# Kernel optimization log

Measured on AMD Instinct MI355X. Metric: run time of the kernel, lower is better.

The kernel has to match this reference:

```python
import jax, jax.numpy as jnp
import numpy as np

R, MAXI, MAXO = 333, 119, 12   # n ROIs, max roi input size, max roi reduced size
E, H = 3328, 8                  # embed dim (concat 3325 + pad 3), heads
HD = E // H                     # 416
CONCAT = 3325
EPS = 1e-5


def _roi_layout():
    """Deterministic synthetic ROI sizes + gather maps for vectorized ragged encode."""
    sizes = 30 + (7 * np.arange(R)) % 90            # per-ROI input widths
    reduced = 8 + np.arange(R) % 5                  # per-ROI output widths
    reduced[332] = 8                                # makes concat+3 divisible by 8
    starts = np.concatenate([[0], np.cumsum(sizes)[:-1]])
    total = int(sizes.sum())                        # 24696
    in_idx = np.minimum(starts[:, None] + np.arange(MAXI)[None, :], total - 1)
    in_mask = (np.arange(MAXI)[None, :] < sizes[:, None]).astype(np.float32)
    out_idx = np.concatenate([i * MAXO + np.arange(reduced[i]) for i in range(R)])
    assert out_idx.shape[0] == CONCAT
    return jnp.asarray(in_idx), jnp.asarray(in_mask), jnp.asarray(out_idx)


def _bn(x, g, b):
    # training-mode BatchNorm1d: biased batch stats (matches torch normalization)
    m = x.mean(0)
    v = x.var(0)
    return (x - m) * jax.lax.rsqrt(v + EPS) * g + b


def _lrelu(x, s):
    return jnp.where(x > 0, x, s * x)


def setup_inputs() -> dict:
    key = jax.random.key(0)
    ks = jax.random.split(key, 16)
    B, TOTAL = 2048, 24696
    f32 = jnp.float32
    return {
        'x': jax.random.normal(ks[0], (B, TOTAL), f32),
        'enc_W': jax.random.normal(ks[1], (R, MAXO, MAXI), f32) * 0.1,
        'enc_b': jax.random.normal(ks[2], (R, MAXO), f32) * 0.02,
        'bn1_g': jnp.ones((CONCAT,), f32),
        'bn1_b': jnp.zeros((CONCAT,), f32),
        'Wqkv': jax.random.normal(ks[3], (3 * E, E), f32) * (1.0 / np.sqrt(E)),
        'bqkv': jnp.zeros((3 * E,), f32),
        'Wo': jax.random.normal(ks[4], (E, E), f32) * (1.0 / np.sqrt(E)),
        'bo': jnp.zeros((E,), f32),
        'W1': jax.random.normal(ks[5], (1024, E), f32) * (1.0 / np.sqrt(E)),
        'b1': jnp.zeros((1024,), f32),
        'bn2_g': jnp.ones((1024,), f32),
        'bn2_b': jnp.zeros((1024,), f32),
        'W2': jax.random.normal(ks[6], (300, 1024), f32) * (1.0 / 32.0),
        'b2': jnp.zeros((300,), f32),
        'Wc': jax.random.normal(ks[7], (180, 300), f32) * 0.06,
        'bc': jnp.zeros((180,), f32),
    }


def reference(x, enc_W, enc_b, bn1_g, bn1_b, Wqkv, bqkv, Wo, bo,
              W1, b1, bn2_g, bn2_b, W2, b2, Wc, bc):
    in_idx, in_mask, out_idx = _roi_layout()
    B = x.shape[0]
    # --- vectorized ragged per-ROI Linear (replaces 333-way python loop) ---
    xp = x[:, in_idx] * in_mask                     # [B, R, MAXI], padded slices
    y = jnp.einsum('bri,roi->bro', xp, enc_W) + enc_b  # [B, R, MAXO]
    y = y.reshape(B, R * MAXO)[:, out_idx]          # ragged concat -> [B, 3325]
    # per-ROI BN+LeakyReLU(0.3) == per-feature on the concat
    y = _lrelu(_bn(y, bn1_g, bn1_b), 0.3)
    y = jnp.pad(y, ((0, 0), (1, 2)))                # F.pad (1, 2) -> [B, 3328]
    # --- MultiheadAttention, seq_len = 1 (input unsqueezed to [1, B, E]) ---
    qkv = y @ Wqkv.T + bqkv                         # [B, 3E]
    q, k, v = jnp.split(qkv, 3, axis=-1)
    q = q.reshape(B, H, 1, HD)
    k = k.reshape(B, H, 1, HD)
    v = v.reshape(B, H, 1, HD)
    s = jnp.einsum('bhqd,bhkd->bhqk', q, k) / jnp.sqrt(jnp.float32(HD))
    a = jax.nn.softmax(s, axis=-1)                  # trivially 1 for L=1, kept faithful
    o = jnp.einsum('bhqk,bhkd->bhqd', a, v).reshape(B, E)
    o = o @ Wo.T + bo
    r = _lrelu(_bn(o @ W1.T + b1, bn2_g, bn2_b), 0.1)
    reg_out = r @ W2.T + b2                         # [B, 300]
    y_pred = jax.nn.softmax(reg_out @ Wc.T + bc, axis=-1)  # [B, 180]
    return reg_out, y_pred
```

## Files before the change

kernel.cpp:

```cpp
#include <hip/hip_runtime.h>
#include <hip/hip_bf16.h>

#define B_      2048
#define R_      333
#define MAXI_   119
#define MAXO_   12
#define CONCAT_ 3325
#define E_      3328
#define TOTAL_  24696
#define HID_    1024
#define NREG_   300
#define NCLS_   180
#define EPS_    1e-5f
#define NSLOT_  128
#define PSTR_   3328
#define NS2_    128

typedef __attribute__((ext_vector_type(8))) short bf16x8;
typedef __attribute__((ext_vector_type(4))) float f32x4;

static __device__ inline unsigned short f2bf_rne(float f) {
  unsigned u;
  __builtin_memcpy(&u, &f, 4);
  u += 0x7fff + ((u >> 16) & 1);
  return (unsigned short)(u >> 16);
}
static __device__ inline float bf2f(unsigned short s) {
  unsigned u = (unsigned)s << 16;
  float f;
  __builtin_memcpy(&f, &u, 4);
  return f;
}

__global__ void layout_kernel(int* __restrict__ starts, int* __restrict__ red_starts) {
  if (threadIdx.x == 0 && blockIdx.x == 0) {
    int s = 0, rs = 0;
    for (int r = 0; r < R_; ++r) {
      starts[r] = s;
      red_starts[r] = rs;
      s += 30 + (7 * r) % 90;
      rs += (r == 332) ? 8 : (8 + r % 5);
    }
  }
}

__device__ __forceinline__ void rowdot_body(
    const float* __restrict__ A, const float* __restrict__ v, const float* __restrict__ b,
    float* __restrict__ out, int N, int K, int jb) {
  int wid = threadIdx.x >> 6, lane = threadIdx.x & 63;
  int j = jb * 4 + wid;
  if (j >= N) return;
  const float* row = A + (size_t)j * K;
  float s = 0.f;
  for (int k = lane; k < K; k += 64) s = fmaf(row[k], v[k], s);
  for (int o = 32; o; o >>= 1) s += __shfl_down(s, o);
  if (lane == 0) out[j] = s + b[j];
}

__device__ __forceinline__ void pack_w_body(const float* __restrict__ enc_W,
                                            const int* __restrict__ starts,
                                            unsigned short* __restrict__ Wpk, int r) {
  int tid = threadIdx.x;
  int kc = tid >> 6, lane = tid & 63;
  int size = 30 + (7 * r) % 90;
  int s8 = starts[r] & 7;
  int oc = lane & 15;
  int k0 = kc * 32 + (lane >> 4) * 8;
  unsigned short o[8];
#pragma unroll
  for (int e = 0; e < 8; ++e) {
    int k = k0 + e - s8;
    float v = 0.f;
    if (oc < MAXO_ && k >= 0 && k < size) v = enc_W[((size_t)r * MAXO_ + oc) * MAXI_ + k];
    o[e] = f2bf_rne(v);
  }
  unsigned short* dst = Wpk + ((size_t)r * 4 + kc) * 512 + lane * 8;
  *(ushort4*)dst = *(ushort4*)&o[0];
  *(ushort4*)(dst + 4) = *(ushort4*)&o[4];
}

__global__ __launch_bounds__(256) void packw_rd1_kernel(
    const float* __restrict__ enc_W, const int* __restrict__ starts,
    unsigned short* __restrict__ Wpk,
    const float* __restrict__ Wo, const float* __restrict__ bv,
    const float* __restrict__ bo, float* __restrict__ t1v) {
  int bid = blockIdx.x;
  if (bid < R_) pack_w_body(enc_W, starts, Wpk, bid);
  else          rowdot_body(Wo, bv, bo, t1v, E_, E_, bid - R_);
}

__device__ __forceinline__ void encode_body(
    const float* __restrict__ x, const unsigned short* __restrict__ Wpk,
    const float* __restrict__ enc_b, const int* __restrict__ starts,
    const int* __restrict__ red_starts,
    unsigned short* __restrict__ yT, float* __restrict__ pS1, float* __restrict__ pS2,
    int r, int bg) {
  int tid = threadIdx.x;
  int wid = tid >> 6, lane = tid & 63;
  int lr = lane & 15, kg = lane >> 4;

  int size = 30 + (7 * r) % 90;
  int red  = (r == 332) ? 8 : (8 + r % 5);
  int st   = starts[r];
  int s8   = st & 7;
  int a0   = st & ~7;
  int rs   = red_starts[r];
  int nkc  = (s8 + size + 31) >> 5;
  int kmax = TOTAL_ - a0;

  bf16x8 wf[4];
  const unsigned short* wp = Wpk + (size_t)r * 2048 + lane * 8;
#pragma unroll
  for (int kc = 0; kc < 4; ++kc) wf[kc] = *(const bf16x8*)(wp + kc * 512);

  float bofs[4];
#pragma unroll
  for (int reg = 0; reg < 4; ++reg) {
    int oc = kg * 4 + reg;
    bofs[reg] = (oc < MAXO_) ? enc_b[r * MAXO_ + oc] : 0.f;
  }

  for (int t = 0; t < 4; ++t) {
    int b0 = bg * 256 + wid * 64 + t * 16;
    const float* xrow = x + (size_t)(b0 + lr) * TOTAL_ + a0;
    f32x4 acc = {0.f, 0.f, 0.f, 0.f};
#pragma unroll
    for (int kc = 0; kc < 4; ++kc) {
      if (kc < nkc) {
        int k0 = kc * 32 + kg * 8;
        if (k0 + 8 > kmax) k0 = kmax - 8;
        float4 v0 = *(const float4*)(xrow + k0);
        float4 v1 = *(const float4*)(xrow + k0 + 4);
        bf16x8 xf;
        xf[0] = (short)f2bf_rne(v0.x); xf[1] = (short)f2bf_rne(v0.y);
        xf[2] = (short)f2bf_rne(v0.z); xf[3] = (short)f2bf_rne(v0.w);
        xf[4] = (short)f2bf_rne(v1.x); xf[5] = (short)f2bf_rne(v1.y);
        xf[6] = (short)f2bf_rne(v1.z); xf[7] = (short)f2bf_rne(v1.w);
        acc = __builtin_amdgcn_mfma_f32_16x16x32_bf16(wf[kc], xf, acc, 0, 0, 0);
      }
    }
    int slot = b0 >> 4;
#pragma unroll
    for (int reg = 0; reg < 4; ++reg) {
      int oc = kg * 4 + reg;
      if (oc < red) {
        float v = acc[reg] + bofs[reg];
        yT[(size_t)(rs + oc) * B_ + b0 + lr] = f2bf_rne(v);
        float a = v, s2 = v * v;
#pragma unroll
        for (int m = 1; m <= 8; m <<= 1) { a += __shfl_xor(a, m); s2 += __shfl_xor(s2, m); }
        if (lr == 0) {
          pS1[slot * PSTR_ + rs + oc] = a;
          pS2[slot * PSTR_ + rs + oc] = s2;
        }
      }
    }
  }
}

#define ENC_NB_ (R_ * 8)
#define NTR_    ((E_ / 64) * (E_ / 64))
#define NC4A_   (HID_ * E_ / 4)
#define NC4B_   (NREG_ * HID_ / 4)
#define NCAST_  ((NC4A_ + NC4B_ + 255) / 256)
__global__ __launch_bounds__(256) void grand_kernel(
    const float* __restrict__ x, const unsigned short* __restrict__ Wpk,
    const float* __restrict__ enc_b, const int* __restrict__ starts,
    const int* __restrict__ red_starts,
    unsigned short* __restrict__ yT, float* __restrict__ pS1, float* __restrict__ pS2,
    const float* __restrict__ Wo, const float* __restrict__ Wv,
    unsigned short* __restrict__ WoT, unsigned short* __restrict__ WvT,
    const float* __restrict__ W1, unsigned short* __restrict__ W1b,
    const float* __restrict__ W2, unsigned short* __restrict__ W2b,
    const float* __restrict__ t1v, const float* __restrict__ b1, float* __restrict__ zbv) {
  __shared__ float tile[64][65];
  int bid = blockIdx.x;
  if (bid < ENC_NB_) {
    encode_body(x, Wpk, enc_b, starts, red_starts, yT, pS1, pS2, bid >> 3, bid & 7);
  } else if (bid < ENC_NB_ + 2 * NTR_) {
    int tb = bid - ENC_NB_;
    int z = tb / NTR_, rem = tb % NTR_;
    const float* in = z ? Wv : Wo;
    unsigned short* out = z ? WvT : WoT;
    int c0 = (rem % 52) * 64, r0 = (rem / 52) * 64;
    int t = threadIdx.x;
    int ci = t & 63, ri0 = t >> 6;
    for (int ri = ri0; ri < 64; ri += 4)
      tile[ri][ci] = in[(size_t)(r0 + ri) * E_ + c0 + ci];
    __syncthreads();
    int rj = t & 63, i0 = t >> 6;
    for (int i = i0; i < 64; i += 4)
      out[(size_t)(c0 + i) * E_ + r0 + rj] = f2bf_rne(tile[rj][i]);
  } else if (bid < ENC_NB_ + 2 * NTR_ + NCAST_) {
    int i = (bid - ENC_NB_ - 2 * NTR_) * 256 + threadIdx.x;
    const float* src; unsigned short* dst; int idx;
    if (i < NC4A_) { src = W1; dst = W1b; idx = i; }
    else if (i < NC4A_ + NC4B_) { src = W2; dst = W2b; idx = i - NC4A_; }
    else return;
    float4 v = ((const float4*)src)[idx];
    ushort4 o;
    o.x = f2bf_rne(v.x); o.y = f2bf_rne(v.y); o.z = f2bf_rne(v.z); o.w = f2bf_rne(v.w);
    ((ushort4*)dst)[idx] = o;
  } else {
    rowdot_body(W1, t1v, b1, zbv, HID_, E_, bid - ENC_NB_ - 2 * NTR_ - NCAST_);
  }
}

template <int KS, bool OUT_BF16>
__device__ __forceinline__ void gemm_body(
    const unsigned short* __restrict__ A, const unsigned short* __restrict__ W,
    float* __restrict__ Cf, unsigned short* __restrict__ Cb,
    int M, int N, int K, int bx, int by, int bz, unsigned short* smem) {
  unsigned short* a_lds = smem;
  unsigned short* b_lds = smem + 8192;
  int tid = threadIdx.x;
  int wid = tid >> 6, lane = tid & 63;
  int wr = wid >> 1, wc = wid & 1;
  int row0 = by * 128, col0 = bx * 128;
  int lr = lane & 15, kg = lane >> 4;
  int Klocal = K / KS;
  int kbase = bz * Klocal;

  int srow = tid >> 2, sk = (tid & 3) * 8;
  const unsigned short* aptr0 = A + (size_t)(row0 + srow) * K + kbase + sk;
  const unsigned short* aptr1 = aptr0 + (size_t)64 * K;
  int bcol0 = col0 + srow;      if (bcol0 > N - 1) bcol0 = N - 1;
  int bcol1 = col0 + 64 + srow; if (bcol1 > N - 1) bcol1 = N - 1;
  const unsigned short* bptr0 = W + (size_t)bcol0 * K + kbase + sk;
  const unsigned short* bptr1 = W + (size_t)bcol1 * K + kbase + sk;

  f32x4 acc[4][4] = {};
  int nk = Klocal >> 5;

#define STAGE_(buf, kc)                                                                             \
  do {                                                                                              \
    __builtin_amdgcn_global_load_lds((const __attribute__((address_space(1))) void*)(aptr0 + (kc)), \
        (__attribute__((address_space(3))) void*)(a_lds + (buf) * 4096 + wid * 512), 16, 0, 0);     \
    __builtin_amdgcn_global_load_lds((const __attribute__((address_space(1))) void*)(aptr1 + (kc)), \
        (__attribute__((address_space(3))) void*)(a_lds + (buf) * 4096 + 2048 + wid * 512), 16, 0, 0); \
    __builtin_amdgcn_global_load_lds((const __attribute__((address_space(1))) void*)(bptr0 + (kc)), \
        (__attribute__((address_space(3))) void*)(b_lds + (buf) * 4096 + wid * 512), 16, 0, 0);     \
    __builtin_amdgcn_global_load_lds((const __attribute__((address_space(1))) void*)(bptr1 + (kc)), \
        (__attribute__((address_space(3))) void*)(b_lds + (buf) * 4096 + 2048 + wid * 512), 16, 0, 0); \
  } while (0)

  STAGE_(0, 0);
  __syncthreads();
  int cur = 0;
  for (int t = 0; t < nk; ++t) {
    if (t + 1 < nk) STAGE_(cur ^ 1, (t + 1) * 32);
    bf16x8 a[4], b[4];
#pragma unroll
    for (int f = 0; f < 4; ++f) {
      a[f] = *(const bf16x8*)(a_lds + cur * 4096 + (wr * 64 + f * 16 + lr) * 32 + kg * 8);
      b[f] = *(const bf16x8*)(b_lds + cur * 4096 + (wc * 64 + f * 16 + lr) * 32 + kg * 8);
    }
#pragma unroll
    for (int i = 0; i < 4; ++i)
#pragma unroll
      for (int j = 0; j < 4; ++j)
        acc[i][j] = __builtin_amdgcn_mfma_f32_16x16x32_bf16(a[i], b[j], acc[i][j], 0, 0, 0);
    __syncthreads();
    cur ^= 1;
  }
#undef STAGE_

#pragma unroll
  for (int j = 0; j < 4; ++j) {
    int ccol = col0 + wc * 64 + j * 16 + lr;
    if (ccol >= N) continue;
#pragma unroll
    for (int i = 0; i < 4; ++i) {
#pragma unroll
      for (int reg = 0; reg < 4; ++reg) {
        int crow = row0 + wr * 64 + i * 16 + kg * 4 + reg;
        float v = acc[i][j][reg];
        if (KS == 1) {
          if (OUT_BF16) Cb[(size_t)crow * N + ccol] = f2bf_rne(v);
          else          Cf[(size_t)crow * N + ccol] = v;
        } else {
          Cf[((size_t)bz * M + crow) * N + ccol] = v;
        }
      }
    }
  }
}

#define WA_NB_ ((E_ / 128) * (HID_ / 128))
__global__ __launch_bounds__(256) void wa_stats_kernel(
    const unsigned short* __restrict__ W1b, const unsigned short* __restrict__ WoT,
    unsigned short* __restrict__ Wa_bf,
    const float* __restrict__ pS1, const float* __restrict__ pS2,
    float* __restrict__ mean, float* __restrict__ rstd) {
  __shared__ __align__(16) unsigned short smem[16384];
  int bid = blockIdx.x;
  if (bid < WA_NB_) {
    gemm_body<1, true>(W1b, WoT, nullptr, Wa_bf, HID_, E_, E_,
                       bid % (E_ / 128), bid / (E_ / 128), 0, smem);
  } else {
    int c = (bid - WA_NB_) * 256 + threadIdx.x;
    if (c >= CONCAT_) return;
    float s = 0.f, s2 = 0.f;
    for (int i = 0; i < NSLOT_; ++i) { s += pS1[i * PSTR_ + c]; s2 += pS2[i * PSTR_ + c]; }
    float m = s / B_;
    float v = s2 / B_ - m * m;
    mean[c] = m;
    rstd[c] = rsqrtf(v + EPS_);
  }
}

#define TR_NB_ ((E_ / 64) * (B_ / 64))
__global__ __launch_bounds__(256) void trans_wb_kernel(
    const unsigned short* __restrict__ yT, const float* __restrict__ mean,
    const float* __restrict__ rstd, const float* __restrict__ g,
    const float* __restrict__ bb, unsigned short* __restrict__ Y,
    const unsigned short* __restrict__ Wa_bf, const unsigned short* __restrict__ WvT,
    unsigned short* __restrict__ Wb_bf) {
  __shared__ __align__(16) unsigned short smem[16384];
  int bid = blockIdx.x;
  if (bid < WA_NB_) {
    gemm_body<1, true>(Wa_bf, WvT, nullptr, Wb_bf, HID_, E_, E_,
                       bid % (E_ / 128), bid / (E_ / 128), 0, smem);
  } else {
    int tb = bid - WA_NB_;
    int cc0 = (tb % 52) * 64, b0 = (tb / 52) * 64;
    float (*tile)[65] = (float(*)[65])smem;
    int t = threadIdx.x;
    int bi = t & 63, ci0 = t >> 6;
    for (int ci = ci0; ci < 64; ci += 4) {
      int c = cc0 + ci - 1;
      float v = 0.f;
      if (c >= 0 && c < CONCAT_) {
        float f = bf2f(yT[(size_t)c * B_ + b0 + bi]);
        v = (f - mean[c]) * rstd[c] * g[c] + bb[c];
        v = v > 0.f ? v : 0.3f * v;
      }
      tile[ci][bi] = v;
    }
    __syncthreads();
    int cj = t & 63, bj0 = t >> 6;
    for (int bj = bj0; bj < 64; bj += 4)
      Y[(size_t)(b0 + bj) * E_ + cc0 + cj] = f2bf_rne(tile[cj][bj]);
  }
}

template <int KS, bool OUT_BF16>
__global__ __launch_bounds__(256) void gemm_kernel(
    const unsigned short* __restrict__ A, const unsigned short* __restrict__ W,
    float* __restrict__ Cf, unsigned short* __restrict__ Cb, int M, int N, int K) {
  __shared__ __align__(16) unsigned short smem[16384];
  gemm_body<KS, OUT_BF16>(A, W, Cf, Cb, M, N, K, blockIdx.x, blockIdx.y, blockIdx.z, smem);
}

__global__ __launch_bounds__(256) void combZ_stats_kernel(
    const float* __restrict__ Cpart, const float* __restrict__ zb,
    float* __restrict__ Z, float* __restrict__ pS, float* __restrict__ pS2) {
  int c = blockIdx.x * 256 + threadIdx.x;
  int ry = blockIdx.y;
  float zbc = zb[c];
  float s1 = 0.f, s2 = 0.f;
  for (int r = ry * 16; r < ry * 16 + 16; ++r) {
    float v = zbc;
#pragma unroll
    for (int z = 0; z < 4; ++z) v += Cpart[((size_t)z * B_ + r) * HID_ + c];
    Z[(size_t)r * HID_ + c] = v;
    s1 += v; s2 = fmaf(v, v, s2);
  }
  pS[ry * HID_ + c] = s1;
  pS2[ry * HID_ + c] = s2;
}

__global__ __launch_bounds__(256) void colstats_final_kernel(
    const float* __restrict__ pS, const float* __restrict__ pS2,
    float* __restrict__ mean, float* __restrict__ rstd) {
  int c = blockIdx.x * 256 + threadIdx.x;
  if (c >= HID_) return;
  float s = 0.f, s2 = 0.f;
  for (int i = 0; i < NS2_; ++i) { s += pS[i * HID_ + c]; s2 += pS2[i * HID_ + c]; }
  float m = s / B_;
  float v = s2 / B_ - m * m;
  mean[c] = m;
  rstd[c] = rsqrtf(v + EPS_);
}

__global__ __launch_bounds__(256) void bn2_apply_kernel(
    const float* __restrict__ Z, const float* __restrict__ mean, const float* __restrict__ rstd,
    const float* __restrict__ g, const float* __restrict__ bb, unsigned short* __restrict__ R) {
  int i = blockIdx.x * 256 + threadIdx.x;
  int c = i & (HID_ - 1);
  float v = (Z[i] - mean[c]) * rstd[c] * g[c] + bb[c];
  v = v > 0.f ? v : 0.1f * v;
  R[i] = f2bf_rne(v);
}

__global__ __launch_bounds__(256) void classifier_kernel(
    const float* __restrict__ Cpart, const float* __restrict__ b2,
    const float* __restrict__ Wc, const float* __restrict__ bc,
    float* __restrict__ reg_out, float* __restrict__ ypred) {
  int b = blockIdx.x;
  __shared__ __align__(16) float rrow[NREG_];
  __shared__ float sl[256];
  int tid = threadIdx.x;
  for (int i = tid; i < NREG_; i += 256) {
    float s = b2[i];
#pragma unroll
    for (int z = 0; z < 4; ++z) s += Cpart[((size_t)z * B_ + b) * NREG_ + i];
    rrow[i] = s;
    reg_out[(size_t)b * NREG_ + i] = s;
  }
  __syncthreads();
  float s = -1e30f;
  if (tid < NCLS_) {
    const float* w = Wc + (size_t)tid * NREG_;
    float acc = 0.f;
    for (int k = 0; k < NREG_; k += 4) {
      float4 wv = *(const float4*)(w + k);
      float4 rv = *(const float4*)(&rrow[k]);
      acc = fmaf(wv.x, rv.x, acc); acc = fmaf(wv.y, rv.y, acc);
      acc = fmaf(wv.z, rv.z, acc); acc = fmaf(wv.w, rv.w, acc);
    }
    s = acc + bc[tid];
  }
  sl[tid] = s;
  __syncthreads();
  for (int o = 128; o > 0; o >>= 1) {
    if (tid < o) sl[tid] = fmaxf(sl[tid], sl[tid + o]);
    __syncthreads();
  }
  float mx = sl[0];
  __syncthreads();
  float e = (tid < NCLS_) ? __expf(s - mx) : 0.f;
  sl[tid] = e;
  __syncthreads();
  for (int o = 128; o > 0; o >>= 1) {
    if (tid < o) sl[tid] += sl[tid + o];
    __syncthreads();
  }
  if (tid < NCLS_) ypred[(size_t)b * NCLS_ + tid] = e / sl[0];
}

extern "C" void kernel_launch(void* const* d_in, const int* in_sizes, int n_in,
                              void* d_out, int out_size, void* d_ws, size_t ws_size,
                              hipStream_t stream) {
  const float* x     = (const float*)d_in[0];
  const float* enc_W = (const float*)d_in[1];
  const float* enc_b = (const float*)d_in[2];
  const float* bn1_g = (const float*)d_in[3];
  const float* bn1_b = (const float*)d_in[4];
  const float* Wqkv  = (const float*)d_in[5];
  const float* bqkv  = (const float*)d_in[6];
  const float* Wo    = (const float*)d_in[7];
  const float* bo    = (const float*)d_in[8];
  const float* W1    = (const float*)d_in[9];
  const float* b1    = (const float*)d_in[10];
  const float* bn2_g = (const float*)d_in[11];
  const float* bn2_b = (const float*)d_in[12];
  const float* W2    = (const float*)d_in[13];
  const float* b2    = (const float*)d_in[14];
  const float* Wc    = (const float*)d_in[15];
  const float* bc    = (const float*)d_in[16];

  char* ws = (char*)d_ws;
  size_t off = 0;
  auto alloc = [&](size_t bytes) -> void* {
    void* p = ws + off;
    off += (bytes + 255) & ~(size_t)255;
    return p;
  };

  unsigned short* yT     = (unsigned short*)alloc((size_t)CONCAT_ * B_ * 2);
  float*          pS1b   = (float*)alloc((size_t)NSLOT_ * PSTR_ * 4);
  float*          pS2b   = (float*)alloc((size_t)NSLOT_ * PSTR_ * 4);
  float*          mean1  = (float*)alloc(CONCAT_ * 4);
  float*          rstd1  = (float*)alloc(CONCAT_ * 4);
  unsigned short* Ybf    = (unsigned short*)alloc((size_t)B_ * E_ * 2);
  unsigned short* Rbf    = (unsigned short*)alloc((size_t)B_ * HID_ * 2);
  unsigned short* WoT_bf = (unsigned short*)alloc((size_t)E_ * E_ * 2);
  unsigned short* WvT_bf = (unsigned short*)alloc((size_t)E_ * E_ * 2);
  unsigned short* W1_bf  = (unsigned short*)alloc((size_t)HID_ * E_ * 2);
  unsigned short* W2_bf  = (unsigned short*)alloc((size_t)NREG_ * HID_ * 2);
  unsigned short* Wa_bf  = (unsigned short*)alloc((size_t)HID_ * E_ * 2);
  unsigned short* Wb_bf  = (unsigned short*)alloc((size_t)HID_ * E_ * 2);
  unsigned short* Wpk    = (unsigned short*)alloc((size_t)R_ * 2048 * 2);
  float*          Cpart  = (float*)alloc((size_t)4 * B_ * HID_ * 4);
  float*          t1v    = (float*)alloc(E_ * 4);
  float*          zbv    = (float*)alloc(HID_ * 4);
  float*          partS  = (float*)alloc((size_t)NS2_ * HID_ * 4);
  float*          partS2 = (float*)alloc((size_t)NS2_ * HID_ * 4);
  float*          mean2  = (float*)alloc(HID_ * 4);
  float*          rstd2  = (float*)alloc(HID_ * 4);
  int*            starts = (int*)alloc(R_ * 4);
  int*            redst  = (int*)alloc(R_ * 4);

  float* Z = (float*)yT;

  layout_kernel<<<1, 1, 0, stream>>>(starts, redst);
  packw_rd1_kernel<<<R_ + E_ / 4, 256, 0, stream>>>(
      enc_W, starts, Wpk, Wo, bqkv + 2 * E_, bo, t1v);
  grand_kernel<<<ENC_NB_ + 2 * NTR_ + NCAST_ + HID_ / 4, 256, 0, stream>>>(
      x, Wpk, enc_b, starts, redst, yT, pS1b, pS2b,
      Wo, Wqkv + (size_t)2 * E_ * E_, WoT_bf, WvT_bf,
      W1, W1_bf, W2, W2_bf, t1v, b1, zbv);
  wa_stats_kernel<<<WA_NB_ + (CONCAT_ + 255) / 256, 256, 0, stream>>>(
      W1_bf, WoT_bf, Wa_bf, pS1b, pS2b, mean1, rstd1);
  trans_wb_kernel<<<WA_NB_ + TR_NB_, 256, 0, stream>>>(
      yT, mean1, rstd1, bn1_g, bn1_b, Ybf, Wa_bf, WvT_bf, Wb_bf);
  gemm_kernel<4, false><<<dim3(HID_ / 128, B_ / 128, 4), 256, 0, stream>>>(
      Ybf, Wb_bf, Cpart, nullptr, B_, HID_, E_);
  combZ_stats_kernel<<<dim3(HID_ / 256, NS2_), 256, 0, stream>>>(Cpart, zbv, Z, partS, partS2);
  colstats_final_kernel<<<(HID_ + 255) / 256, 256, 0, stream>>>(partS, partS2, mean2, rstd2);
  bn2_apply_kernel<<<(B_ * HID_) / 256, 256, 0, stream>>>(Z, mean2, rstd2, bn2_g, bn2_b, Rbf);
  gemm_kernel<4, false><<<dim3((NREG_ + 127) / 128, B_ / 128, 4), 256, 0, stream>>>(
      Rbf, W2_bf, Cpart, nullptr, B_, NREG_, HID_);
  float* reg_out = (float*)d_out;
  classifier_kernel<<<B_, 256, 0, stream>>>(
      Cpart, b2, Wc, bc, reg_out, reg_out + (size_t)B_ * NREG_);
}
```

Baseline: 351.0 us.

## Reschedule kernel stages to overlap encode with weight-fold GEMM and split-K Wb

Weight transposes, casts and packing move into one prep kernel. The ROI encode now runs in the same launch as the Wa = W1·Wo fold GEMM, so the memory-bound encode overlaps the compute-bound GEMM. The encode no longer writes per-slot partial BN statistics; instead the column statistics are recomputed by reading yT back, in the same launch as a split-K (2-way) Wb GEMM. A later kernel sums the two Wb partials to bf16 alongside the transpose. The trade is an extra read of yT and extra fp32 partial traffic for Wb, in exchange for better concurrency and fewer partial-stat writes.

```diff
diff --git a/kernel.cpp b/kernel.cpp
--- a/kernel.cpp
+++ b/kernel.cpp
@@ -12,8 +12,6 @@
 #define NREG_   300
 #define NCLS_   180
 #define EPS_    1e-5f
-#define NSLOT_  128
-#define PSTR_   3328
 #define NS2_    128
 
 typedef __attribute__((ext_vector_type(8))) short bf16x8;
@@ -79,22 +77,55 @@
   *(ushort4*)(dst + 4) = *(ushort4*)&o[4];
 }
 
-__global__ __launch_bounds__(256) void packw_rd1_kernel(
+#define NTR_    ((E_ / 64) * (E_ / 64))
+#define NC4A_   (HID_ * E_ / 4)
+#define NC4B_   (NREG_ * HID_ / 4)
+#define NCAST_  ((NC4A_ + NC4B_ + 255) / 256)
+__global__ __launch_bounds__(256) void prep_kernel(
+    const float* __restrict__ Wo, const float* __restrict__ Wv,
+    unsigned short* __restrict__ WoT, unsigned short* __restrict__ WvT,
+    const float* __restrict__ W1, unsigned short* __restrict__ W1b,
+    const float* __restrict__ W2, unsigned short* __restrict__ W2b,
+    const float* __restrict__ bv, const float* __restrict__ bo, float* __restrict__ t1v,
     const float* __restrict__ enc_W, const int* __restrict__ starts,
-    unsigned short* __restrict__ Wpk,
-    const float* __restrict__ Wo, const float* __restrict__ bv,
-    const float* __restrict__ bo, float* __restrict__ t1v) {
+    unsigned short* __restrict__ Wpk) {
+  __shared__ float tile[64][65];
   int bid = blockIdx.x;
-  if (bid < R_) pack_w_body(enc_W, starts, Wpk, bid);
-  else          rowdot_body(Wo, bv, bo, t1v, E_, E_, bid - R_);
+  if (bid < 2 * NTR_) {
+    int z = bid / NTR_, rem = bid % NTR_;
+    const float* in = z ? Wv : Wo;
+    unsigned short* out = z ? WvT : WoT;
+    int c0 = (rem % 52) * 64, r0 = (rem / 52) * 64;
+    int t = threadIdx.x;
+    int ci = t & 63, ri0 = t >> 6;
+    for (int ri = ri0; ri < 64; ri += 4)
+      tile[ri][ci] = in[(size_t)(r0 + ri) * E_ + c0 + ci];
+    __syncthreads();
+    int rj = t & 63, i0 = t >> 6;
+    for (int i = i0; i < 64; i += 4)
+      out[(size_t)(c0 + i) * E_ + r0 + rj] = f2bf_rne(tile[rj][i]);
+  } else if (bid < 2 * NTR_ + NCAST_) {
+    int i = (bid - 2 * NTR_) * 256 + threadIdx.x;
+    const float* src; unsigned short* dst; int idx;
+    if (i < NC4A_) { src = W1; dst = W1b; idx = i; }
+    else if (i < NC4A_ + NC4B_) { src = W2; dst = W2b; idx = i - NC4A_; }
+    else return;
+    float4 v = ((const float4*)src)[idx];
+    ushort4 o;
+    o.x = f2bf_rne(v.x); o.y = f2bf_rne(v.y); o.z = f2bf_rne(v.z); o.w = f2bf_rne(v.w);
+    ((ushort4*)dst)[idx] = o;
+  } else if (bid < 2 * NTR_ + NCAST_ + E_ / 4) {
+    rowdot_body(Wo, bv, bo, t1v, E_, E_, bid - 2 * NTR_ - NCAST_);
+  } else {
+    pack_w_body(enc_W, starts, Wpk, bid - 2 * NTR_ - NCAST_ - E_ / 4);
+  }
 }
 
 __device__ __forceinline__ void encode_body(
     const float* __restrict__ x, const unsigned short* __restrict__ Wpk,
     const float* __restrict__ enc_b, const int* __restrict__ starts,
     const int* __restrict__ red_starts,
-    unsigned short* __restrict__ yT, float* __restrict__ pS1, float* __restrict__ pS2,
-    int r, int bg) {
+    unsigned short* __restrict__ yT, int r, int bg) {
   int tid = threadIdx.x;
   int wid = tid >> 6, lane = tid & 63;
   int lr = lane & 15, kg = lane >> 4;
@@ -139,70 +170,12 @@
         acc = __builtin_amdgcn_mfma_f32_16x16x32_bf16(wf[kc], xf, acc, 0, 0, 0);
       }
     }
-    int slot = b0 >> 4;
 #pragma unroll
     for (int reg = 0; reg < 4; ++reg) {
       int oc = kg * 4 + reg;
-      if (oc < red) {
-        float v = acc[reg] + bofs[reg];
-        yT[(size_t)(rs + oc) * B_ + b0 + lr] = f2bf_rne(v);
-        float a = v, s2 = v * v;
-#pragma unroll
-        for (int m = 1; m <= 8; m <<= 1) { a += __shfl_xor(a, m); s2 += __shfl_xor(s2, m); }
-        if (lr == 0) {
-          pS1[slot * PSTR_ + rs + oc] = a;
-          pS2[slot * PSTR_ + rs + oc] = s2;
-        }
-      }
-    }
-  }
-}
-
-#define ENC_NB_ (R_ * 8)
-#define NTR_    ((E_ / 64) * (E_ / 64))
-#define NC4A_   (HID_ * E_ / 4)
-#define NC4B_   (NREG_ * HID_ / 4)
-#define NCAST_  ((NC4A_ + NC4B_ + 255) / 256)
-__global__ __launch_bounds__(256) void grand_kernel(
-    const float* __restrict__ x, const unsigned short* __restrict__ Wpk,
-    const float* __restrict__ enc_b, const int* __restrict__ starts,
-    const int* __restrict__ red_starts,
-    unsigned short* __restrict__ yT, float* __restrict__ pS1, float* __restrict__ pS2,
-    const float* __restrict__ Wo, const float* __restrict__ Wv,
-    unsigned short* __restrict__ WoT, unsigned short* __restrict__ WvT,
-    const float* __restrict__ W1, unsigned short* __restrict__ W1b,
-    const float* __restrict__ W2, unsigned short* __restrict__ W2b,
-    const float* __restrict__ t1v, const float* __restrict__ b1, float* __restrict__ zbv) {
-  __shared__ float tile[64][65];
-  int bid = blockIdx.x;
-  if (bid < ENC_NB_) {
-    encode_body(x, Wpk, enc_b, starts, red_starts, yT, pS1, pS2, bid >> 3, bid & 7);
-  } else if (bid < ENC_NB_ + 2 * NTR_) {
-    int tb = bid - ENC_NB_;
-    int z = tb / NTR_, rem = tb % NTR_;
-    const float* in = z ? Wv : Wo;
-    unsigned short* out = z ? WvT : WoT;
-    int c0 = (rem % 52) * 64, r0 = (rem / 52) * 64;
-    int t = threadIdx.x;
-    int ci = t & 63, ri0 = t >> 6;
-    for (int ri = ri0; ri < 64; ri += 4)
-      tile[ri][ci] = in[(size_t)(r0 + ri) * E_ + c0 + ci];
-    __syncthreads();
-    int rj = t & 63, i0 = t >> 6;
-    for (int i = i0; i < 64; i += 4)
-      out[(size_t)(c0 + i) * E_ + r0 + rj] = f2bf_rne(tile[rj][i]);
-  } else if (bid < ENC_NB_ + 2 * NTR_ + NCAST_) {
-    int i = (bid - ENC_NB_ - 2 * NTR_) * 256 + threadIdx.x;
-    const float* src; unsigned short* dst; int idx;
-    if (i < NC4A_) { src = W1; dst = W1b; idx = i; }
-    else if (i < NC4A_ + NC4B_) { src = W2; dst = W2b; idx = i - NC4A_; }
-    else return;
-    float4 v = ((const float4*)src)[idx];
-    ushort4 o;
-    o.x = f2bf_rne(v.x); o.y = f2bf_rne(v.y); o.z = f2bf_rne(v.z); o.w = f2bf_rne(v.w);
-    ((ushort4*)dst)[idx] = o;
-  } else {
-    rowdot_body(W1, t1v, b1, zbv, HID_, E_, bid - ENC_NB_ - 2 * NTR_ - NCAST_);
+      if (oc < red)
+        yT[(size_t)(rs + oc) * B_ + b0 + lr] = f2bf_rne(acc[reg] + bofs[reg]);
+    }
   }
 }
 
@@ -286,45 +259,80 @@
   }
 }
 
-#define WA_NB_ ((E_ / 128) * (HID_ / 128))
-__global__ __launch_bounds__(256) void wa_stats_kernel(
+#define WA_NB_  ((E_ / 128) * (HID_ / 128))
+#define ENC_NB_ (R_ * 8)
+__global__ __launch_bounds__(256) void mega_kernel(
+    const float* __restrict__ x, const unsigned short* __restrict__ Wpk,
+    const float* __restrict__ enc_b, const int* __restrict__ starts,
+    const int* __restrict__ red_starts, unsigned short* __restrict__ yT,
     const unsigned short* __restrict__ W1b, const unsigned short* __restrict__ WoT,
     unsigned short* __restrict__ Wa_bf,
-    const float* __restrict__ pS1, const float* __restrict__ pS2,
-    float* __restrict__ mean, float* __restrict__ rstd) {
+    const float* __restrict__ W1, const float* __restrict__ t1v,
+    const float* __restrict__ b1, float* __restrict__ zbv) {
   __shared__ __align__(16) unsigned short smem[16384];
   int bid = blockIdx.x;
   if (bid < WA_NB_) {
     gemm_body<1, true>(W1b, WoT, nullptr, Wa_bf, HID_, E_, E_,
                        bid % (E_ / 128), bid / (E_ / 128), 0, smem);
+  } else if (bid < WA_NB_ + ENC_NB_) {
+    int eb = bid - WA_NB_;
+    encode_body(x, Wpk, enc_b, starts, red_starts, yT, eb >> 3, eb & 7);
   } else {
-    int c = (bid - WA_NB_) * 256 + threadIdx.x;
-    if (c >= CONCAT_) return;
+    rowdot_body(W1, t1v, b1, zbv, HID_, E_, bid - WA_NB_ - ENC_NB_);
+  }
+}
+
+#define WB2_NB_ (WA_NB_ * 2)
+#define ST_NB_  ((CONCAT_ + 15) / 16)
+__global__ __launch_bounds__(256) void wb_stats_kernel(
+    const unsigned short* __restrict__ Wa_bf, const unsigned short* __restrict__ WvT,
+    float* __restrict__ Cpart,
+    const unsigned short* __restrict__ yT, float* __restrict__ mean, float* __restrict__ rstd) {
+  __shared__ __align__(16) unsigned short smem[16384];
+  int bid = blockIdx.x;
+  if (bid < WB2_NB_) {
+    int z = bid / WA_NB_, rem = bid % WA_NB_;
+    gemm_body<2, false>(Wa_bf, WvT, Cpart, nullptr, HID_, E_, E_,
+                        rem % (E_ / 128), rem / (E_ / 128), z, smem);
+  } else {
+    int tb = bid - WB2_NB_;
+    int t = threadIdx.x;
+    int f = tb * 16 + (t >> 4);
+    int j = t & 15;
+    if (f >= CONCAT_) return;
+    const unsigned short* p = yT + (size_t)f * B_ + j * 128;
     float s = 0.f, s2 = 0.f;
-    for (int i = 0; i < NSLOT_; ++i) { s += pS1[i * PSTR_ + c]; s2 += pS2[i * PSTR_ + c]; }
-    float m = s / B_;
-    float v = s2 / B_ - m * m;
-    mean[c] = m;
-    rstd[c] = rsqrtf(v + EPS_);
+#pragma unroll
+    for (int i = 0; i < 16; ++i) {
+      bf16x8 v = *(const bf16x8*)(p + i * 8);
+#pragma unroll
+      for (int e = 0; e < 8; ++e) {
+        float xv = bf2f((unsigned short)v[e]);
+        s += xv; s2 = fmaf(xv, xv, s2);
+      }
+    }
+#pragma unroll
+    for (int m = 1; m <= 8; m <<= 1) { s += __shfl_xor(s, m); s2 += __shfl_xor(s2, m); }
+    if (j == 0) {
+      float mm = s / B_;
+      float var = s2 / B_ - mm * mm;
+      mean[f] = mm;
+      rstd[f] = rsqrtf(var + EPS_);
+    }
   }
 }
 
 #define TR_NB_ ((E_ / 64) * (B_ / 64))
-__global__ __launch_bounds__(256) void trans_wb_kernel(
+#define CWB_NB_ (HID_ * E_ / 4 / 256)
+__global__ __launch_bounds__(256) void trans_comb_kernel(
     const unsigned short* __restrict__ yT, const float* __restrict__ mean,
     const float* __restrict__ rstd, const float* __restrict__ g,
     const float* __restrict__ bb, unsigned short* __restrict__ Y,
-    const unsigned short* __restrict__ Wa_bf, const unsigned short* __restrict__ WvT,
-    unsigned short* __restrict__ Wb_bf) {
-  __shared__ __align__(16) unsigned short smem[16384];
+    const float* __restrict__ Cpart, unsigned short* __restrict__ Wb_bf) {
+  __shared__ float tile[64][65];
   int bid = blockIdx.x;
-  if (bid < WA_NB_) {
-    gemm_body<1, true>(Wa_bf, WvT, nullptr, Wb_bf, HID_, E_, E_,
-                       bid % (E_ / 128), bid / (E_ / 128), 0, smem);
-  } else {
-    int tb = bid - WA_NB_;
-    int cc0 = (tb % 52) * 64, b0 = (tb / 52) * 64;
-    float (*tile)[65] = (float(*)[65])smem;
+  if (bid < TR_NB_) {
+    int cc0 = (bid % 52) * 64, b0 = (bid / 52) * 64;
     int t = threadIdx.x;
     int bi = t & 63, ci0 = t >> 6;
     for (int ci = ci0; ci < 64; ci += 4) {
@@ -341,6 +349,16 @@
     int cj = t & 63, bj0 = t >> 6;
     for (int bj = bj0; bj < 64; bj += 4)
       Y[(size_t)(b0 + bj) * E_ + cc0 + cj] = f2bf_rne(tile[cj][bj]);
+  } else {
+    int i4 = (bid - TR_NB_) * 256 + threadIdx.x;
+    const int MN4 = HID_ * E_ / 4;
+    if (i4 >= MN4) return;
+    float4 a = ((const float4*)Cpart)[i4];
+    float4 b = ((const float4*)(Cpart + (size_t)HID_ * E_))[i4];
+    ushort4 o;
+    o.x = f2bf_rne(a.x + b.x); o.y = f2bf_rne(a.y + b.y);
+    o.z = f2bf_rne(a.z + b.z); o.w = f2bf_rne(a.w + b.w);
+    ((ushort4*)Wb_bf)[i4] = o;
   }
 }
 
@@ -469,8 +487,6 @@
   };
 
   unsigned short* yT     = (unsigned short*)alloc((size_t)CONCAT_ * B_ * 2);
-  float*          pS1b   = (float*)alloc((size_t)NSLOT_ * PSTR_ * 4);
-  float*          pS2b   = (float*)alloc((size_t)NSLOT_ * PSTR_ * 4);
   float*          mean1  = (float*)alloc(CONCAT_ * 4);
   float*          rstd1  = (float*)alloc(CONCAT_ * 4);
   unsigned short* Ybf    = (unsigned short*)alloc((size_t)B_ * E_ * 2);
@@ -495,16 +511,15 @@
   float* Z = (float*)yT;
 
   layout_kernel<<<1, 1, 0, stream>>>(starts, redst);
-  packw_rd1_kernel<<<R_ + E_ / 4, 256, 0, stream>>>(
-      enc_W, starts, Wpk, Wo, bqkv + 2 * E_, bo, t1v);
-  grand_kernel<<<ENC_NB_ + 2 * NTR_ + NCAST_ + HID_ / 4, 256, 0, stream>>>(
-      x, Wpk, enc_b, starts, redst, yT, pS1b, pS2b,
+  prep_kernel<<<2 * NTR_ + NCAST_ + E_ / 4 + R_, 256, 0, stream>>>(
       Wo, Wqkv + (size_t)2 * E_ * E_, WoT_bf, WvT_bf,
-      W1, W1_bf, W2, W2_bf, t1v, b1, zbv);
-  wa_stats_kernel<<<WA_NB_ + (CONCAT_ + 255) / 256, 256, 0, stream>>>(
-      W1_bf, WoT_bf, Wa_bf, pS1b, pS2b, mean1, rstd1);
-  trans_wb_kernel<<<WA_NB_ + TR_NB_, 256, 0, stream>>>(
-      yT, mean1, rstd1, bn1_g, bn1_b, Ybf, Wa_bf, WvT_bf, Wb_bf);
+      W1, W1_bf, W2, W2_bf, bqkv + 2 * E_, bo, t1v, enc_W, starts, Wpk);
+  mega_kernel<<<WA_NB_ + ENC_NB_ + HID_ / 4, 256, 0, stream>>>(
+      x, Wpk, enc_b, starts, redst, yT, W1_bf, WoT_bf, Wa_bf, W1, t1v, b1, zbv);
+  wb_stats_kernel<<<WB2_NB_ + ST_NB_, 256, 0, stream>>>(
+      Wa_bf, WvT_bf, Cpart, yT, mean1, rstd1);
+  trans_comb_kernel<<<TR_NB_ + CWB_NB_, 256, 0, stream>>>(
+      yT, mean1, rstd1, bn1_g, bn1_b, Ybf, Cpart, Wb_bf);
   gemm_kernel<4, false><<<dim3(HID_ / 128, B_ / 128, 4), 256, 0, stream>>>(
       Ybf, Wb_bf, Cpart, nullptr, B_, HID_, E_);
   combZ_stats_kernel<<<dim3(HID_ / 256, NS2_), 256, 0, stream>>>(Cpart, zbv, Z, partS, partS2);
```

After: 313.6 us. -10.7%, faster.
